# Optimization experiments

Hardware: AMD Instinct MI355X
Metric: run time of the kernel (lower is better)

The kernel has to match this reference:

```python
import jax, jax.numpy as jnp
import numpy as np

D = 256
RANK = 64
H = 8
DH = D // H
TOPK = 32  # top-k survivors per query row
NEG = -1e9


def lowrank(x, u, v):
    # x:[...,d] @ u:[d,rank] @ v:[rank,d]
    return (x @ u) @ v


def setup_inputs() -> dict:
    key = jax.random.key(0)
    ks = jax.random.split(key, 13)
    s_u = 1.0 / np.sqrt(D)
    s_v = 1.0 / np.sqrt(RANK)

    def pu(k):
        return jax.random.normal(k, (D, RANK), jnp.float32) * s_u

    def pv(k):
        return jax.random.normal(k, (RANK, D), jnp.float32) * s_v

    return {
        "x": jax.random.normal(ks[0], (2, 2048, D), jnp.float32),
        "ne_u": pu(ks[1]), "ne_v": pv(ks[2]),
        "wq_u": pu(ks[3]), "wq_v": pv(ks[4]),
        "wk_u": pu(ks[5]), "wk_v": pv(ks[6]),
        "wv_u": pu(ks[7]), "wv_v": pv(ks[8]),
        "wo_u": pu(ks[9]), "wo_v": pv(ks[10]),
        "es_u": pu(ks[11]), "es_v": pv(ks[12]),
    }


def reference(x, ne_u, ne_v, wq_u, wq_v, wk_u, wk_v, wv_u, wv_v, wo_u, wo_v, es_u, es_v):
    B, N, _ = x.shape
    # node embedding (low-rank projection)
    h = lowrank(x, ne_u, ne_v)  # [B,N,d]

    # low-rank multi-head Q/K/V
    def heads(t):  # [B,N,d] -> [B,H,N,dh]
        return t.reshape(B, N, H, DH).transpose(0, 2, 1, 3)

    q = heads(lowrank(h, wq_u, wq_v))
    k = heads(lowrank(h, wk_u, wk_v))
    v = heads(lowrank(h, wv_u, wv_v))

    scores = jnp.einsum("bhnd,bhmd->bhnm", q, k) / jnp.sqrt(jnp.float32(DH))
    # top-k sparsification per query row
    kth = jax.lax.top_k(scores, TOPK)[0][..., -1:]  # [B,H,N,1]
    masked = jnp.where(scores >= kth, scores, NEG)
    attn = jax.nn.softmax(masked, axis=-1)  # [B,H,N,N]

    out = jnp.einsum("bhnm,bhmd->bhnd", attn, v)  # [B,H,N,dh]
    out = out.transpose(0, 2, 1, 3).reshape(B, N, D)
    h2 = lowrank(out, wo_u, wo_v)  # output projection

    # edge scores -> adjacency with sigmoid + zero diagonal epilogue
    el = lowrank(h2, es_u, es_v)  # [B,N,d]
    adjacency = jax.nn.sigmoid(jnp.einsum("bnd,bmd->bnm", el, el))
    adjacency = adjacency * (1.0 - jnp.eye(N, dtype=adjacency.dtype))
    return adjacency, attn
```

## Files before the change

kernel.cpp:

```cpp
#include <hip/hip_runtime.h>
#include <hip/hip_bf16.h>
#include <cstdint>
#include <cstddef>

#define ATTN_OFF (2u*2048u*2048u)
#define SLOTS 48
#define DELTA 1e-3f
#define MAXB 16
#define CCAP 96

typedef __attribute__((ext_vector_type(8))) short bf16x8;
typedef __attribute__((ext_vector_type(4))) float f32x4;

__device__ __forceinline__ unsigned short bf16_hi(float f) {
  __hip_bfloat16 h = __float2bfloat16(f);
  return *(unsigned short*)&h;
}
__device__ __forceinline__ float bf16_val(unsigned short u) {
  __hip_bfloat16 h = *(__hip_bfloat16*)&u;
  return __bfloat162float(h);
}

__global__ __launch_bounds__(256) void fused_qkv_kernel(
    const float* __restrict__ x, const float* __restrict__ ne_u,
    const float* __restrict__ ne_v, const float* __restrict__ wq_u,
    const float* __restrict__ wq_v, const float* __restrict__ wk_u,
    const float* __restrict__ wk_v, const float* __restrict__ wv_u,
    const float* __restrict__ wv_v, double* __restrict__ qd,
    double* __restrict__ kd, unsigned short* __restrict__ qh,
    unsigned short* __restrict__ ql, unsigned short* __restrict__ kh,
    unsigned short* __restrict__ kl, float* __restrict__ v) {
  __shared__ double xm[4][64];
  __shared__ double hrow[4][256];
  __shared__ double mid2[4][64];

  int tid = threadIdx.x;
  int rr = tid >> 6;
  int j  = tid & 63;
  int row = blockIdx.x * 4 + rr;
  int b = row >> 11, m = row & 2047;
  const double INV = 0.17677669529663688110021109052621;

  const float* xr = x + (size_t)row * 256;
  {
    double a0 = 0, a1 = 0, a2 = 0, a3 = 0;
#pragma unroll 8
    for (int k4 = 0; k4 < 64; ++k4) {
      int kk = k4 * 4;
      a0 = fma((double)xr[kk + 0], (double)ne_u[(kk + 0) * 64 + j], a0);
      a1 = fma((double)xr[kk + 1], (double)ne_u[(kk + 1) * 64 + j], a1);
      a2 = fma((double)xr[kk + 2], (double)ne_u[(kk + 2) * 64 + j], a2);
      a3 = fma((double)xr[kk + 3], (double)ne_u[(kk + 3) * 64 + j], a3);
    }
    xm[rr][j] = (a0 + a1) + (a2 + a3);
  }
  __syncthreads();

#pragma unroll
  for (int cc = 0; cc < 4; ++cc) {
    int col = j + 64 * cc;
    double o0 = 0, o1 = 0, o2 = 0, o3 = 0;
#pragma unroll 4
    for (int r4 = 0; r4 < 16; ++r4) {
      int r = r4 * 4;
      o0 = fma(xm[rr][r + 0], (double)ne_v[(r + 0) * 256 + col], o0);
      o1 = fma(xm[rr][r + 1], (double)ne_v[(r + 1) * 256 + col], o1);
      o2 = fma(xm[rr][r + 2], (double)ne_v[(r + 2) * 256 + col], o2);
      o3 = fma(xm[rr][r + 3], (double)ne_v[(r + 3) * 256 + col], o3);
    }
    hrow[rr][col] = (o0 + o1) + (o2 + o3);
  }
  __syncthreads();

  for (int p = 0; p < 3; ++p) {
    const float* pu = (p == 0) ? wq_u : (p == 1) ? wk_u : wv_u;
    const float* pw = (p == 0) ? wq_v : (p == 1) ? wk_v : wv_v;

    double a0 = 0, a1 = 0, a2 = 0, a3 = 0;
#pragma unroll 8
    for (int k4 = 0; k4 < 64; ++k4) {
      int kk = k4 * 4;
      a0 = fma(hrow[rr][kk + 0], (double)pu[(kk + 0) * 64 + j], a0);
      a1 = fma(hrow[rr][kk + 1], (double)pu[(kk + 1) * 64 + j], a1);
      a2 = fma(hrow[rr][kk + 2], (double)pu[(kk + 2) * 64 + j], a2);
      a3 = fma(hrow[rr][kk + 3], (double)pu[(kk + 3) * 64 + j], a3);
    }
    mid2[rr][j] = (a0 + a1) + (a2 + a3);
    __syncthreads();

#pragma unroll
    for (int cc = 0; cc < 4; ++cc) {
      int col = j + 64 * cc;
      double o0 = 0, o1 = 0, o2 = 0, o3 = 0;
#pragma unroll 4
      for (int r4 = 0; r4 < 16; ++r4) {
        int r = r4 * 4;
        o0 = fma(mid2[rr][r + 0], (double)pw[(r + 0) * 256 + col], o0);
        o1 = fma(mid2[rr][r + 1], (double)pw[(r + 1) * 256 + col], o1);
        o2 = fma(mid2[rr][r + 2], (double)pw[(r + 2) * 256 + col], o2);
        o3 = fma(mid2[rr][r + 3], (double)pw[(r + 3) * 256 + col], o3);
      }
      double o = (o0 + o1) + (o2 + o3);
      if (p == 2) {
        v[(size_t)row * 256 + col] = (float)o;
      } else {
        int hh = col >> 5, d = col & 31;
        size_t haddr = (((size_t)(b * 8 + hh)) * 2048 + m) * 32 + d;
        if (p == 0) {
          qd[(size_t)row * 256 + col] = o;
          float f = (float)(o * INV);
          unsigned short hi = bf16_hi(f);
          float lof = f - bf16_val(hi);
          qh[haddr] = hi;
          ql[haddr] = bf16_hi(lof);
        } else {
          kd[(size_t)row * 256 + col] = o;
          float f = (float)o;
          unsigned short hi = bf16_hi(f);
          float lof = f - bf16_val(hi);
          kh[haddr] = hi;
          kl[haddr] = bf16_hi(lof);
        }
      }
    }
    __syncthreads();
  }
}

__global__ __launch_bounds__(512, 4) void attn_kernel(
    const unsigned short* __restrict__ qh, const unsigned short* __restrict__ ql,
    const unsigned short* __restrict__ kh, const unsigned short* __restrict__ kl,
    const double* __restrict__ qd, const double* __restrict__ kd,
    float* __restrict__ attn, float* __restrict__ pval,
    unsigned short* __restrict__ pidx) {
  __shared__ unsigned hist[16][256];
  __shared__ float cand[16][CCAP];
  __shared__ float sval[16][SLOTS];
  __shared__ unsigned short scol[16][SLOTS];
  __shared__ float rowmax_s[16][8];
  __shared__ float zpart_s[16][8];
  __shared__ float mx_s[16];
  __shared__ float kth_s[16];
  __shared__ float zinv_s[16];
  __shared__ int   kB_s[16];
  __shared__ unsigned kneed_s[16];
  __shared__ unsigned ccnt[16];
  __shared__ unsigned scnt[16];
  __shared__ unsigned chi_s[16];
  __shared__ unsigned bcnt[16];
  __shared__ unsigned short bidx[16][MAXB];
  __shared__ unsigned short bkeep[16][MAXB];
  __shared__ double bs64[16][MAXB];

  int tid = threadIdx.x;
  int bx  = blockIdx.x;
  int slab = bx >> 7;
  int rowtile = bx & 127;
  int b = slab >> 3, hh = slab & 7;
  int w = tid >> 6;
  int l = tid & 63;
  int g = l >> 4;
  int li = l & 15;
  const double INV64 = 0.17677669529663688110021109052621;

  size_t qoff = (((size_t)slab * 2048 + rowtile * 16 + li) * 32) + g * 8;
  bf16x8 a_hi = *(const bf16x8*)(qh + qoff);
  bf16x8 a_lo = *(const bf16x8*)(ql + qoff);

  float s[16][4];
  size_t kbase = ((size_t)slab * 2048 + w * 256 + li) * 32 + g * 8;
#pragma unroll
  for (int tt = 0; tt < 16; ++tt) {
    bf16x8 b_hi = *(const bf16x8*)(kh + kbase + (size_t)tt * 512);
    bf16x8 b_lo = *(const bf16x8*)(kl + kbase + (size_t)tt * 512);
    f32x4 acc = {0.f, 0.f, 0.f, 0.f};
    acc = __builtin_amdgcn_mfma_f32_16x16x32_bf16(a_hi, b_hi, acc, 0, 0, 0);
    acc = __builtin_amdgcn_mfma_f32_16x16x32_bf16(a_hi, b_lo, acc, 0, 0, 0);
    acc = __builtin_amdgcn_mfma_f32_16x16x32_bf16(a_lo, b_hi, acc, 0, 0, 0);
#pragma unroll
    for (int reg = 0; reg < 4; ++reg) s[tt][reg] = acc[reg];
  }

  for (int i = tid; i < 16 * 256; i += 512) ((unsigned*)hist)[i] = 0u;
  for (int i = tid; i < 16 * SLOTS; i += 512) {
    ((float*)sval)[i] = 0.0f;
    ((unsigned short*)scol)[i] = 0;
  }
  if (tid < 16) {
    ccnt[tid] = 0u; scnt[tid] = 0u; chi_s[tid] = 0u; bcnt[tid] = 0u;
    kth_s[tid] = -1e30f; kB_s[tid] = -1;
  }
  size_t prow0 = ((size_t)slab * 2048 + rowtile * 16);
  {
    float lmx[4];
#pragma unroll
    for (int reg = 0; reg < 4; ++reg) {
      float m = s[0][reg];
#pragma unroll
      for (int tt = 1; tt < 16; ++tt) m = fmaxf(m, s[tt][reg]);
      lmx[reg] = m;
    }
#pragma unroll
    for (int off = 1; off < 16; off <<= 1) {
#pragma unroll
      for (int reg = 0; reg < 4; ++reg)
        lmx[reg] = fmaxf(lmx[reg], __shfl_xor(lmx[reg], (unsigned)off, 16));
    }
    if (li == 0) {
#pragma unroll
      for (int reg = 0; reg < 4; ++reg) rowmax_s[4 * g + reg][w] = lmx[reg];
    }
  }
  __syncthreads();

  if (tid < 16) {
    float m = rowmax_s[tid][0];
#pragma unroll
    for (int i = 1; i < 8; ++i) m = fmaxf(m, rowmax_s[tid][i]);
    mx_s[tid] = m;
  }
  __syncthreads();

#pragma unroll
  for (int reg = 0; reg < 4; ++reg) {
    int rloc = 4 * g + reg;
    float mx = mx_s[rloc];
#pragma unroll
    for (int tt = 0; tt < 16; ++tt) {
      int bb = (int)((mx - s[tt][reg]) * 16.0f);
      bb = bb > 255 ? 255 : bb;
      atomicAdd(&hist[rloc][bb], 1u);
    }
  }
  __syncthreads();

  if (w < 4) {
    int rloc = w * 4 + g;
    unsigned cnt16 = 0;
#pragma unroll
    for (int i = 0; i < 16; ++i) cnt16 += hist[rloc][li * 16 + i];
    unsigned pre = cnt16;
#pragma unroll
    for (int off = 1; off < 16; off <<= 1) {
      unsigned t = __shfl_up(pre, (unsigned)off, 16);
      if (li >= off) pre += t;
    }
    unsigned excl = pre - cnt16;
    bool flag = (excl < 32u) && (pre >= 32u);
    unsigned long long bal = __ballot(flag);
    unsigned seg = (unsigned)((bal >> (g * 16)) & 0xFFFFull);
    if (flag) {
      int src = __ffs(seg) - 1;
      if (li == src) {
        unsigned cum = excl;
        int B = 255; unsigned cb = 0;
#pragma unroll
        for (int i = 0; i < 16; ++i) {
          unsigned hv = hist[rloc][li * 16 + i];
          if (cum < 32u && cum + hv >= 32u) { B = li * 16 + i; cb = cum; }
          cum += hv;
        }
        kB_s[rloc] = B;
        kneed_s[rloc] = 32u - cb;
      }
    }
  }
  __syncthreads();

#pragma unroll
  for (int reg = 0; reg < 4; ++reg) {
    int rloc = 4 * g + reg;
    float mx = mx_s[rloc];
    int kB = kB_s[rloc];
#pragma unroll
    for (int tt = 0; tt < 16; ++tt) {
      int bb = (int)((mx - s[tt][reg]) * 16.0f);
      bb = bb > 255 ? 255 : bb;
      if (bb == kB) {
        unsigned slot = atomicAdd(&ccnt[rloc], 1u);
        if (slot < (unsigned)CCAP) cand[rloc][slot] = s[tt][reg];
      }
    }
  }
  __syncthreads();

  if (w < 4) {
    int rloc = w * 4 + g;
    unsigned n0 = ccnt[rloc];
    n0 = n0 > (unsigned)CCAP ? (unsigned)CCAP : n0;
    unsigned need = kneed_s[rloc];
    if (need > n0) need = n0;
    for (unsigned ci = (unsigned)li; ci < n0; ci += 16u) {
      float x = cand[rloc][ci];
      unsigned r = 0;
      for (unsigned jj = 0; jj < n0; ++jj) {
        float y = cand[rloc][jj];
        r += (y > x || (y == x && jj < ci)) ? 1u : 0u;
      }
      if (r == need - 1u) kth_s[rloc] = x;
    }
  }
  __syncthreads();

#pragma unroll
  for (int reg = 0; reg < 4; ++reg) {
    int rloc = 4 * g + reg;
    float kth = kth_s[rloc];
    unsigned cnt = 0;
#pragma unroll
    for (int tt = 0; tt < 16; ++tt) {
      float v = s[tt][reg];
      if (v > kth + DELTA) {
        ++cnt;
      } else if (!(v < kth - DELTA)) {
        unsigned slot = atomicAdd(&bcnt[rloc], 1u);
        if (slot < (unsigned)MAXB)
          bidx[rloc][slot] = (unsigned short)(w * 256 + tt * 16 + li);
      }
    }
#pragma unroll
    for (int off = 1; off < 16; off <<= 1)
      cnt += (unsigned)__shfl_xor((int)cnt, off, 16);
    if (li == 0) atomicAdd(&chi_s[rloc], cnt);
  }
  __syncthreads();

  if (w < 4) {
    int rloc = w * 4 + g;
    unsigned bn = bcnt[rloc];
    bn = bn > (unsigned)MAXB ? (unsigned)MAXB : bn;
    const double* qrow =
        qd + ((size_t)(b * 2048 + rowtile * 16 + rloc)) * 256 + hh * 32;
    for (unsigned ci = (unsigned)li; ci < bn; ci += 16u) {
      int m = bidx[rloc][ci];
      const double* krow = kd + ((size_t)(b * 2048 + m)) * 256 + hh * 32;
      double acc = 0.0;
#pragma unroll 8
      for (int d = 0; d < 32; ++d) acc = fma(qrow[d], krow[d], acc);
      bs64[rloc][ci] = acc * INV64;
    }
    unsigned need2 = 32u - chi_s[rloc];
    for (unsigned ci = (unsigned)li; ci < bn; ci += 16u) {
      double x = bs64[rloc][ci];
      unsigned r = 0;
      for (unsigned jj = 0; jj < bn; ++jj)
        r += (bs64[rloc][jj] > x) ? 1u : 0u;
      bkeep[rloc][ci] = (r < need2) ? 1 : 0;
    }
  }
  __syncthreads();

  {
    float zs[4];
#pragma unroll
    for (int reg = 0; reg < 4; ++reg) {
      int rloc = 4 * g + reg;
      float mx = mx_s[rloc], kth = kth_s[rloc];
      unsigned bn = bcnt[rloc];
      bn = bn > (unsigned)MAXB ? (unsigned)MAXB : bn;
      float z = 0.0f;
#pragma unroll
      for (int tt = 0; tt < 16; ++tt) {
        float v = s[tt][reg];
        bool keep;
        if (v > kth + DELTA) {
          keep = true;
        } else if (v < kth - DELTA) {
          keep = false;
        } else {
          unsigned short col = (unsigned short)(w * 256 + tt * 16 + li);
          keep = (v >= kth);
          for (unsigned jj = 0; jj < bn; ++jj) {
            if (bidx[rloc][jj] == col) { keep = bkeep[rloc][jj] != 0; break; }
          }
        }
        float p = keep ? __expf(v - mx) : 0.0f;
        s[tt][reg] = p;
        z += p;
      }
      zs[reg] = z;
    }
#pragma unroll
    for (int off = 1; off < 16; off <<= 1) {
#pragma unroll
      for (int reg = 0; reg < 4; ++reg)
        zs[reg] += __shfl_xor(zs[reg], (unsigned)off, 16);
    }
    if (li == 0) {
#pragma unroll
      for (int reg = 0; reg < 4; ++reg) zpart_s[4 * g + reg][w] = zs[reg];
    }
  }
  __syncthreads();

  if (tid < 16) {
    float z = 0.0f;
#pragma unroll
    for (int i = 0; i < 8; ++i) z += zpart_s[tid][i];
    zinv_s[tid] = 1.0f / z;
  }
  __syncthreads();

#pragma unroll
  for (int reg = 0; reg < 4; ++reg) {
    int rloc = 4 * g + reg;
    float rz = zinv_s[rloc];
#pragma unroll
    for (int tt = 0; tt < 16; ++tt) {
      float p = s[tt][reg];
      if (p > 0.0f) {
        unsigned slot = atomicAdd(&scnt[rloc], 1u);
        if (slot < (unsigned)SLOTS) {
          sval[rloc][slot] = p * rz;
          scol[rloc][slot] = (unsigned short)(w * 256 + tt * 16 + li);
        }
      }
    }
  }

  float* base = attn + prow0 * 2048;
  f32x4 z4 = {0.f, 0.f, 0.f, 0.f};
#pragma unroll
  for (int it = 0; it < 16; ++it)
    __builtin_nontemporal_store(z4, ((f32x4*)base) + tid + 512 * it);

  __syncthreads();

  for (int e = tid; e < 16 * SLOTS; e += 512) {
    int rr = e / SLOTS, ii = e % SLOTS;
    float p = sval[rr][ii];
    unsigned short c = scol[rr][ii];
    if (p != 0.0f) base[(size_t)rr * 2048 + c] = p;
    pval[prow0 * SLOTS + e] = p;
    pidx[prow0 * SLOTS + e] = c;
  }
}

__global__ __launch_bounds__(256) void pv_wo_es_kernel(
    const float* __restrict__ pval, const unsigned short* __restrict__ pidx,
    const float* __restrict__ v,
    const float* __restrict__ wo_u, const float* __restrict__ wo_v,
    const float* __restrict__ es_u, const float* __restrict__ es_v,
    unsigned short* __restrict__ elh, unsigned short* __restrict__ ell) {
  __shared__ float svals[8][8][SLOTS];
  __shared__ unsigned short sidx[8][8][SLOTS];
  __shared__ float outr[8][256];
  __shared__ float mid[8][64];
  __shared__ float h2r[8][256];

  int tid = threadIdx.x;
  int bb = blockIdx.x >> 8;
  int rg = blockIdx.x & 255;
  int n0 = rg * 8;

  for (int e = tid; e < 8 * 8 * SLOTS; e += 256) {
    int rr = e / (8 * SLOTS);
    int rem = e % (8 * SLOTS);
    int hh = rem / SLOTS, ii = rem % SLOTS;
    size_t srow = ((size_t)(bb * 8 + hh) * 2048 + n0 + rr) * SLOTS + ii;
    svals[rr][hh][ii] = pval[srow];
    sidx[rr][hh][ii] = pidx[srow];
  }
  __syncthreads();

  {
    int d = tid, hh = d >> 5;
    const float* vb = v + (size_t)bb * 2048 * 256 + d;
    for (int r = 0; r < 8; ++r) {
      float acc = 0.f;
#pragma unroll 4
      for (int i = 0; i < SLOTS; ++i) {
        float p = svals[r][hh][i];
        int m = sidx[r][hh][i];
        acc = fmaf(p, vb[(size_t)m * 256], acc);
      }
      outr[r][d] = acc;
    }
  }
  __syncthreads();

  {
    int j = tid & 63, rb = tid >> 6;
    for (int r = rb; r < 8; r += 4) {
      float a0 = 0, a1 = 0, a2 = 0, a3 = 0;
#pragma unroll 8
      for (int k4 = 0; k4 < 64; ++k4) {
        int k = k4 * 4;
        a0 = fmaf(outr[r][k + 0], wo_u[(k + 0) * 64 + j], a0);
        a1 = fmaf(outr[r][k + 1], wo_u[(k + 1) * 64 + j], a1);
        a2 = fmaf(outr[r][k + 2], wo_u[(k + 2) * 64 + j], a2);
        a3 = fmaf(outr[r][k + 3], wo_u[(k + 3) * 64 + j], a3);
      }
      mid[r][j] = (a0 + a1) + (a2 + a3);
    }
  }
  __syncthreads();

  {
    int c = tid;
    for (int r = 0; r < 8; ++r) {
      float a0 = 0, a1 = 0, a2 = 0, a3 = 0;
#pragma unroll 4
      for (int k4 = 0; k4 < 16; ++k4) {
        int k = k4 * 4;
        a0 = fmaf(mid[r][k + 0], wo_v[(k + 0) * 256 + c], a0);
        a1 = fmaf(mid[r][k + 1], wo_v[(k + 1) * 256 + c], a1);
        a2 = fmaf(mid[r][k + 2], wo_v[(k + 2) * 256 + c], a2);
        a3 = fmaf(mid[r][k + 3], wo_v[(k + 3) * 256 + c], a3);
      }
      h2r[r][c] = (a0 + a1) + (a2 + a3);
    }
  }
  __syncthreads();

  {
    int j = tid & 63, rb = tid >> 6;
    for (int r = rb; r < 8; r += 4) {
      float a0 = 0, a1 = 0, a2 = 0, a3 = 0;
#pragma unroll 8
      for (int k4 = 0; k4 < 64; ++k4) {
        int k = k4 * 4;
        a0 = fmaf(h2r[r][k + 0], es_u[(k + 0) * 64 + j], a0);
        a1 = fmaf(h2r[r][k + 1], es_u[(k + 1) * 64 + j], a1);
        a2 = fmaf(h2r[r][k + 2], es_u[(k + 2) * 64 + j], a2);
        a3 = fmaf(h2r[r][k + 3], es_u[(k + 3) * 64 + j], a3);
      }
      mid[r][j] = (a0 + a1) + (a2 + a3);
    }
  }
  __syncthreads();

  {
    int c = tid;
    for (int r = 0; r < 8; ++r) {
      float a0 = 0, a1 = 0, a2 = 0, a3 = 0;
#pragma unroll 4
      for (int k4 = 0; k4 < 16; ++k4) {
        int k = k4 * 4;
        a0 = fmaf(mid[r][k + 0], es_v[(k + 0) * 256 + c], a0);
        a1 = fmaf(mid[r][k + 1], es_v[(k + 1) * 256 + c], a1);
        a2 = fmaf(mid[r][k + 2], es_v[(k + 2) * 256 + c], a2);
        a3 = fmaf(mid[r][k + 3], es_v[(k + 3) * 256 + c], a3);
      }
      float o = (a0 + a1) + (a2 + a3);
      size_t addr = ((size_t)(bb * 2048 + n0 + r)) * 256 + c;
      unsigned short hi = bf16_hi(o);
      elh[addr] = hi;
      ell[addr] = bf16_hi(o - bf16_val(hi));
    }
  }
}

__global__ __launch_bounds__(256) void adj_mfma_kernel(
    const unsigned short* __restrict__ elh, const unsigned short* __restrict__ ell,
    float* __restrict__ adj) {
  int tid = threadIdx.x;
  int l = tid & 63, w = tid >> 6;
  int li = l & 15, g = l >> 4;
  int b = blockIdx.z, rt = blockIdx.y, ct = blockIdx.x;

  int arow = rt * 64 + w * 16 + li;
  size_t abase = ((size_t)(b * 2048 + arow)) * 256 + g * 8;
  size_t bbase = ((size_t)(b * 2048 + ct * 64 + li)) * 256 + g * 8;

  f32x4 acc0 = {0.f, 0.f, 0.f, 0.f};
  f32x4 acc1 = {0.f, 0.f, 0.f, 0.f};
  f32x4 acc2 = {0.f, 0.f, 0.f, 0.f};
  f32x4 acc3 = {0.f, 0.f, 0.f, 0.f};

#pragma unroll
  for (int kc = 0; kc < 8; ++kc) {
    bf16x8 a_hi = *(const bf16x8*)(elh + abase + kc * 32);
    bf16x8 a_lo = *(const bf16x8*)(ell + abase + kc * 32);
#pragma unroll
    for (int t = 0; t < 4; ++t) {
      bf16x8 b_hi = *(const bf16x8*)(elh + bbase + (size_t)t * 16 * 256 + kc * 32);
      bf16x8 b_lo = *(const bf16x8*)(ell + bbase + (size_t)t * 16 * 256 + kc * 32);
      f32x4* pa = (t == 0) ? &acc0 : (t == 1) ? &acc1 : (t == 2) ? &acc2 : &acc3;
      *pa = __builtin_amdgcn_mfma_f32_16x16x32_bf16(a_hi, b_hi, *pa, 0, 0, 0);
      *pa = __builtin_amdgcn_mfma_f32_16x16x32_bf16(a_hi, b_lo, *pa, 0, 0, 0);
      *pa = __builtin_amdgcn_mfma_f32_16x16x32_bf16(a_lo, b_hi, *pa, 0, 0, 0);
    }
  }

  int orow0 = rt * 64 + w * 16 + g * 4;
#pragma unroll
  for (int t = 0; t < 4; ++t) {
    f32x4 a = (t == 0) ? acc0 : (t == 1) ? acc1 : (t == 2) ? acc2 : acc3;
    int cg = ct * 64 + t * 16 + li;
#pragma unroll
    for (int i = 0; i < 4; ++i) {
      int rg = orow0 + i;
      float sg = 1.0f / (1.0f + __expf(-a[i]));
      if (rg == cg) sg = 0.0f;
      adj[((size_t)b * 2048 + rg) * 2048 + cg] = sg;
    }
  }
}

extern "C" void kernel_launch(void* const* d_in, const int* in_sizes, int n_in,
                              void* d_out, int out_size, void* d_ws,
                              size_t ws_size, hipStream_t stream) {
  const float* x    = (const float*)d_in[0];
  const float* ne_u = (const float*)d_in[1];
  const float* ne_v = (const float*)d_in[2];
  const float* wq_u = (const float*)d_in[3];
  const float* wq_v = (const float*)d_in[4];
  const float* wk_u = (const float*)d_in[5];
  const float* wk_v = (const float*)d_in[6];
  const float* wv_u = (const float*)d_in[7];
  const float* wv_v = (const float*)d_in[8];
  const float* wo_u = (const float*)d_in[9];
  const float* wo_v = (const float*)d_in[10];
  const float* es_u = (const float*)d_in[11];
  const float* es_v = (const float*)d_in[12];

  float* adj  = (float*)d_out;
  float* attn = adj + (size_t)ATTN_OFF;

  char* ws = (char*)d_ws;
  double* qd = (double*)(ws);
  double* kd = (double*)(ws + ((size_t)8  << 20));
  unsigned short* qh = (unsigned short*)(ws + ((size_t)16 << 20));
  unsigned short* ql = (unsigned short*)(ws + ((size_t)18 << 20));
  unsigned short* kh = (unsigned short*)(ws + ((size_t)20 << 20));
  unsigned short* kl = (unsigned short*)(ws + ((size_t)22 << 20));
  float* v    = (float*)(ws + ((size_t)24 << 20));
  float* pval = (float*)(ws + ((size_t)28 << 20));
  unsigned short* pidx = (unsigned short*)(ws + ((size_t)35 << 20));
  unsigned short* elh = (unsigned short*)(ws + ((size_t)8  << 20));
  unsigned short* ell = (unsigned short*)(ws + ((size_t)10 << 20));

  fused_qkv_kernel<<<1024, 256, 0, stream>>>(
      x, ne_u, ne_v, wq_u, wq_v, wk_u, wk_v, wv_u, wv_v,
      qd, kd, qh, ql, kh, kl, v);

  attn_kernel<<<2048, 512, 0, stream>>>(qh, ql, kh, kl, qd, kd, attn, pval, pidx);
  pv_wo_es_kernel<<<512, 256, 0, stream>>>(pval, pidx, v, wo_u, wo_v,
                                           es_u, es_v, elh, ell);

  adj_mfma_kernel<<<dim3(32, 32, 2), 256, 0, stream>>>(elh, ell, adj);
}
```

Measured before the change: 414.1 us.

## Prefilter top-k histogram with adaptive range and compact softmax over survivors

Before building the histogram, each row counts scores within 1 and 2 of the row max and picks a bin scale and cutoff. The histogram shrinks to 64 bins and only scores above the cutoff do atomic adds. Survivors are written straight into the slot arrays during thresholding, so the normaliser and exponentials are computed over at most 48 survivors per row instead of all 2048 register scores, and two block syncs disappear. Half the block zero-fills the attention tile while the other half computes the normaliser. Binning behaviour changes for rows whose scores fall outside the chosen window, which risks missing candidates if the adaptive scale is mis-set.

```diff
diff --git a/kernel.cpp b/kernel.cpp
--- a/kernel.cpp
+++ b/kernel.cpp
@@ -133,15 +133,18 @@
     const double* __restrict__ qd, const double* __restrict__ kd,
     float* __restrict__ attn, float* __restrict__ pval,
     unsigned short* __restrict__ pidx) {
-  __shared__ unsigned hist[16][256];
+  __shared__ unsigned hist[16][64];
   __shared__ float cand[16][CCAP];
   __shared__ float sval[16][SLOTS];
   __shared__ unsigned short scol[16][SLOTS];
   __shared__ float rowmax_s[16][8];
-  __shared__ float zpart_s[16][8];
+  __shared__ unsigned c1_s[16][8];
+  __shared__ unsigned c2_s[16][8];
   __shared__ float mx_s[16];
   __shared__ float kth_s[16];
   __shared__ float zinv_s[16];
+  __shared__ float scale_s[16];
+  __shared__ float thr_s[16];
   __shared__ int   kB_s[16];
   __shared__ unsigned kneed_s[16];
   __shared__ unsigned ccnt[16];
@@ -149,6 +152,7 @@
   __shared__ unsigned chi_s[16];
   __shared__ unsigned bcnt[16];
   __shared__ unsigned short bidx[16][MAXB];
+  __shared__ float bval[16][MAXB];
   __shared__ unsigned short bkeep[16][MAXB];
   __shared__ double bs64[16][MAXB];
 
@@ -181,11 +185,7 @@
     for (int reg = 0; reg < 4; ++reg) s[tt][reg] = acc[reg];
   }
 
-  for (int i = tid; i < 16 * 256; i += 512) ((unsigned*)hist)[i] = 0u;
-  for (int i = tid; i < 16 * SLOTS; i += 512) {
-    ((float*)sval)[i] = 0.0f;
-    ((unsigned short*)scol)[i] = 0;
-  }
+  for (int i = tid; i < 16 * 64; i += 512) ((unsigned*)hist)[i] = 0u;
   if (tid < 16) {
     ccnt[tid] = 0u; scnt[tid] = 0u; chi_s[tid] = 0u; bcnt[tid] = 0u;
     kth_s[tid] = -1e30f; kB_s[tid] = -1;
@@ -221,31 +221,79 @@
   }
   __syncthreads();
 
+  {
+    unsigned cc1[4], cc2[4];
+#pragma unroll
+    for (int reg = 0; reg < 4; ++reg) {
+      float mx = mx_s[4 * g + reg];
+      float t1 = mx - 1.0f, t2 = mx - 2.0f;
+      unsigned a = 0, c = 0;
+#pragma unroll
+      for (int tt = 0; tt < 16; ++tt) {
+        float v = s[tt][reg];
+        a += (v >= t1) ? 1u : 0u;
+        c += (v >= t2) ? 1u : 0u;
+      }
+      cc1[reg] = a; cc2[reg] = c;
+    }
+#pragma unroll
+    for (int off = 1; off < 16; off <<= 1) {
+#pragma unroll
+      for (int reg = 0; reg < 4; ++reg) {
+        cc1[reg] += (unsigned)__shfl_xor((int)cc1[reg], off, 16);
+        cc2[reg] += (unsigned)__shfl_xor((int)cc2[reg], off, 16);
+      }
+    }
+    if (li == 0) {
+#pragma unroll
+      for (int reg = 0; reg < 4; ++reg) {
+        c1_s[4 * g + reg][w] = cc1[reg];
+        c2_s[4 * g + reg][w] = cc2[reg];
+      }
+    }
+  }
+  __syncthreads();
+
+  if (tid < 16) {
+    unsigned t1 = 0, t2 = 0;
+#pragma unroll
+    for (int i = 0; i < 8; ++i) { t1 += c1_s[tid][i]; t2 += c2_s[tid][i]; }
+    float scale, thr;
+    if (t1 >= 32u)      { scale = 64.0f; thr = mx_s[tid] - 1.0f; }
+    else if (t2 >= 32u) { scale = 32.0f; thr = mx_s[tid] - 2.0f; }
+    else                { scale = 4.0f;  thr = -1e30f; }
+    scale_s[tid] = scale; thr_s[tid] = thr;
+  }
+  __syncthreads();
+
 #pragma unroll
   for (int reg = 0; reg < 4; ++reg) {
     int rloc = 4 * g + reg;
-    float mx = mx_s[rloc];
+    float mx = mx_s[rloc], thr = thr_s[rloc], sc = scale_s[rloc];
 #pragma unroll
     for (int tt = 0; tt < 16; ++tt) {
-      int bb = (int)((mx - s[tt][reg]) * 16.0f);
-      bb = bb > 255 ? 255 : bb;
-      atomicAdd(&hist[rloc][bb], 1u);
+      float v = s[tt][reg];
+      if (v >= thr) {
+        int bb = (int)((mx - v) * sc);
+        bb = bb > 63 ? 63 : bb;
+        atomicAdd(&hist[rloc][bb], 1u);
+      }
     }
   }
   __syncthreads();
 
   if (w < 4) {
     int rloc = w * 4 + g;
-    unsigned cnt16 = 0;
-#pragma unroll
-    for (int i = 0; i < 16; ++i) cnt16 += hist[rloc][li * 16 + i];
-    unsigned pre = cnt16;
+    unsigned cnt4 = 0;
+#pragma unroll
+    for (int i = 0; i < 4; ++i) cnt4 += hist[rloc][li * 4 + i];
+    unsigned pre = cnt4;
 #pragma unroll
     for (int off = 1; off < 16; off <<= 1) {
       unsigned t = __shfl_up(pre, (unsigned)off, 16);
       if (li >= off) pre += t;
     }
-    unsigned excl = pre - cnt16;
+    unsigned excl = pre - cnt4;
     bool flag = (excl < 32u) && (pre >= 32u);
     unsigned long long bal = __ballot(flag);
     unsigned seg = (unsigned)((bal >> (g * 16)) & 0xFFFFull);
@@ -253,11 +301,11 @@
       int src = __ffs(seg) - 1;
       if (li == src) {
         unsigned cum = excl;
-        int B = 255; unsigned cb = 0;
-#pragma unroll
-        for (int i = 0; i < 16; ++i) {
-          unsigned hv = hist[rloc][li * 16 + i];
-          if (cum < 32u && cum + hv >= 32u) { B = li * 16 + i; cb = cum; }
+        int B = 63; unsigned cb = 0;
+#pragma unroll
+        for (int i = 0; i < 4; ++i) {
+          unsigned hv = hist[rloc][li * 4 + i];
+          if (cum < 32u && cum + hv >= 32u) { B = li * 4 + i; cb = cum; }
           cum += hv;
         }
         kB_s[rloc] = B;
@@ -270,15 +318,18 @@
 #pragma unroll
   for (int reg = 0; reg < 4; ++reg) {
     int rloc = 4 * g + reg;
-    float mx = mx_s[rloc];
+    float mx = mx_s[rloc], thr = thr_s[rloc], sc = scale_s[rloc];
     int kB = kB_s[rloc];
 #pragma unroll
     for (int tt = 0; tt < 16; ++tt) {
-      int bb = (int)((mx - s[tt][reg]) * 16.0f);
-      bb = bb > 255 ? 255 : bb;
-      if (bb == kB) {
-        unsigned slot = atomicAdd(&ccnt[rloc], 1u);
-        if (slot < (unsigned)CCAP) cand[rloc][slot] = s[tt][reg];
+      float v = s[tt][reg];
+      if (v >= thr) {
+        int bb = (int)((mx - v) * sc);
+        bb = bb > 63 ? 63 : bb;
+        if (bb == kB) {
+          unsigned slot = atomicAdd(&ccnt[rloc], 1u);
+          if (slot < (unsigned)CCAP) cand[rloc][slot] = v;
+        }
       }
     }
   }
@@ -312,10 +363,17 @@
       float v = s[tt][reg];
       if (v > kth + DELTA) {
         ++cnt;
+        unsigned slot = atomicAdd(&scnt[rloc], 1u);
+        if (slot < (unsigned)SLOTS) {
+          sval[rloc][slot] = v;
+          scol[rloc][slot] = (unsigned short)(w * 256 + tt * 16 + li);
+        }
       } else if (!(v < kth - DELTA)) {
         unsigned slot = atomicAdd(&bcnt[rloc], 1u);
-        if (slot < (unsigned)MAXB)
+        if (slot < (unsigned)MAXB) {
           bidx[rloc][slot] = (unsigned short)(w * 256 + tt * 16 + li);
+          bval[rloc][slot] = v;
+        }
       }
     }
 #pragma unroll
@@ -345,92 +403,49 @@
       unsigned r = 0;
       for (unsigned jj = 0; jj < bn; ++jj)
         r += (bs64[rloc][jj] > x) ? 1u : 0u;
-      bkeep[rloc][ci] = (r < need2) ? 1 : 0;
-    }
-  }
-  __syncthreads();
-
-  {
-    float zs[4];
-#pragma unroll
-    for (int reg = 0; reg < 4; ++reg) {
-      int rloc = 4 * g + reg;
-      float mx = mx_s[rloc], kth = kth_s[rloc];
-      unsigned bn = bcnt[rloc];
-      bn = bn > (unsigned)MAXB ? (unsigned)MAXB : bn;
-      float z = 0.0f;
-#pragma unroll
-      for (int tt = 0; tt < 16; ++tt) {
-        float v = s[tt][reg];
-        bool keep;
-        if (v > kth + DELTA) {
-          keep = true;
-        } else if (v < kth - DELTA) {
-          keep = false;
-        } else {
-          unsigned short col = (unsigned short)(w * 256 + tt * 16 + li);
-          keep = (v >= kth);
-          for (unsigned jj = 0; jj < bn; ++jj) {
-            if (bidx[rloc][jj] == col) { keep = bkeep[rloc][jj] != 0; break; }
-          }
-        }
-        float p = keep ? __expf(v - mx) : 0.0f;
-        s[tt][reg] = p;
-        z += p;
-      }
-      zs[reg] = z;
-    }
-#pragma unroll
-    for (int off = 1; off < 16; off <<= 1) {
-#pragma unroll
-      for (int reg = 0; reg < 4; ++reg)
-        zs[reg] += __shfl_xor(zs[reg], (unsigned)off, 16);
-    }
-    if (li == 0) {
-#pragma unroll
-      for (int reg = 0; reg < 4; ++reg) zpart_s[4 * g + reg][w] = zs[reg];
-    }
-  }
-  __syncthreads();
-
-  if (tid < 16) {
-    float z = 0.0f;
-#pragma unroll
-    for (int i = 0; i < 8; ++i) z += zpart_s[tid][i];
-    zinv_s[tid] = 1.0f / z;
-  }
-  __syncthreads();
-
-#pragma unroll
-  for (int reg = 0; reg < 4; ++reg) {
-    int rloc = 4 * g + reg;
-    float rz = zinv_s[rloc];
-#pragma unroll
-    for (int tt = 0; tt < 16; ++tt) {
-      float p = s[tt][reg];
-      if (p > 0.0f) {
+      if (r < need2) {
         unsigned slot = atomicAdd(&scnt[rloc], 1u);
         if (slot < (unsigned)SLOTS) {
-          sval[rloc][slot] = p * rz;
-          scol[rloc][slot] = (unsigned short)(w * 256 + tt * 16 + li);
+          sval[rloc][slot] = bval[rloc][ci];
+          scol[rloc][slot] = bidx[rloc][ci];
         }
       }
     }
   }
+  __syncthreads();
 
   float* base = attn + prow0 * 2048;
-  f32x4 z4 = {0.f, 0.f, 0.f, 0.f};
-#pragma unroll
-  for (int it = 0; it < 16; ++it)
-    __builtin_nontemporal_store(z4, ((f32x4*)base) + tid + 512 * it);
-
+  if (w < 4) {
+    int rloc = w * 4 + g;
+    unsigned n = scnt[rloc];
+    n = n > (unsigned)SLOTS ? (unsigned)SLOTS : n;
+    float mx = mx_s[rloc];
+    float z = 0.0f;
+    for (unsigned i = (unsigned)li; i < n; i += 16u)
+      z += __expf(sval[rloc][i] - mx);
+#pragma unroll
+    for (int off = 1; off < 16; off <<= 1) z += __shfl_xor(z, (unsigned)off, 16);
+    if (li == 0) zinv_s[rloc] = 1.0f / z;
+  } else {
+    int t2 = tid - 256;
+    f32x4 z4 = {0.f, 0.f, 0.f, 0.f};
+#pragma unroll
+    for (int it = 0; it < 32; ++it)
+      __builtin_nontemporal_store(z4, ((f32x4*)base) + t2 + 256 * it);
+  }
   __syncthreads();
 
   for (int e = tid; e < 16 * SLOTS; e += 512) {
     int rr = e / SLOTS, ii = e % SLOTS;
-    float p = sval[rr][ii];
-    unsigned short c = scol[rr][ii];
-    if (p != 0.0f) base[(size_t)rr * 2048 + c] = p;
+    unsigned n = scnt[rr];
+    n = n > (unsigned)SLOTS ? (unsigned)SLOTS : n;
+    float p = 0.0f;
+    unsigned short c = 0;
+    if ((unsigned)ii < n) {
+      c = scol[rr][ii];
+      p = __expf(sval[rr][ii] - mx_s[rr]) * zinv_s[rr];
+      base[(size_t)rr * 2048 + c] = p;
+    }
     pval[prow0 * SLOTS + e] = p;
     pidx[prow0 * SLOTS + e] = c;
   }
```

Measured after the change: 395.7 us. 4.5% less time.
